# Kernel tuning notes

Hardware: AMD Instinct MI355X
Metric: run time of the kernel (lower is better)

Reference implementation:

```python
import jax, jax.numpy as jnp
import numpy as np

D_MODEL = 1024
NUM_ATOMS = 16384
TEMPERATURE = 1.0
NEG_INF = -1e9


def setup_inputs() -> dict:
    key = jax.random.key(0)
    kx, kd, km = jax.random.split(key, 3)
    x = jax.random.normal(kx, (4, 2048, D_MODEL), dtype=jnp.float32)
    # xavier_uniform for [num_atoms, d_model]
    limit = float(np.sqrt(6.0 / (NUM_ATOMS + D_MODEL)))
    dictionary = jax.random.uniform(
        kd, (NUM_ATOMS, D_MODEL), dtype=jnp.float32, minval=-limit, maxval=limit
    )
    mask = jax.random.randint(km, (4, 2048, NUM_ATOMS), 0, 2, dtype=jnp.int32)
    return {"x": x, "dictionary": dictionary, "mask": mask}


def reference(x, dictionary, mask):
    # scores: [b, s, num_atoms]
    scores = jnp.einsum("bsd,ad->bsa", x, dictionary)
    m = mask.astype(scores.dtype)
    scores = scores * m + (1.0 - m) * NEG_INF
    weights = jax.nn.softmax(scores / TEMPERATURE, axis=-1)
    reconstruction = jnp.einsum("bsa,ad->bsd", weights, dictionary)
    argmax_indices = jnp.argmax(scores, axis=-1)
    return reconstruction, argmax_indices
```

## Files before the change

### kernel.cpp

```cpp
#include <hip/hip_runtime.h>

#define NTOK   8192
#define DMODEL 1024
#define NATOM  16384

typedef _Float16 half8  __attribute__((ext_vector_type(8)));
typedef _Float16 half4_t __attribute__((ext_vector_type(4)));
typedef float    f32x4  __attribute__((ext_vector_type(4)));

#define GLOAD_LDS16(gsrc, ldst) \
  __builtin_amdgcn_global_load_lds((const __attribute__((address_space(1))) unsigned int*)(gsrc), \
                                   (__attribute__((address_space(3))) unsigned int*)(ldst), 16, 0, 0)

__global__ void cvt_f32_f16(const float* __restrict__ in, _Float16* __restrict__ out, int n4) {
  int i = blockIdx.x * 256 + threadIdx.x;
  if (i >= n4) return;
  float4 v = ((const float4*)in)[i];
  half4_t h;
  h[0] = (_Float16)v.x; h[1] = (_Float16)v.y; h[2] = (_Float16)v.z; h[3] = (_Float16)v.w;
  ((half4_t*)out)[i] = h;
}

__global__ void transpose_dict(const float* __restrict__ dict,
                               _Float16* __restrict__ Dh, _Float16* __restrict__ dT) {
  __shared__ _Float16 tile[64][68];
  int a0 = blockIdx.x * 64;
  int d0 = blockIdx.y * 64;
  int tid = threadIdx.x;
  int c = tid & 63;
  int r0 = tid >> 6;
  #pragma unroll
  for (int i = 0; i < 16; i++) {
    int r = r0 + i * 4;
    _Float16 h = (_Float16)dict[(size_t)(a0 + r) * DMODEL + d0 + c];
    tile[r][c] = h;
    Dh[(size_t)(a0 + r) * DMODEL + d0 + c] = h;
  }
  __syncthreads();
  #pragma unroll
  for (int i = 0; i < 16; i++) {
    int rd = r0 + i * 4;
    dT[(size_t)(d0 + rd) * NATOM + a0 + c] = tile[c][rd];
  }
}

__global__ void zero_lsum(float* __restrict__ lsum) {
  lsum[blockIdx.x * 256 + threadIdx.x] = 0.0f;
}

__device__ __forceinline__ void stage_ab(const _Float16* __restrict__ A,
                                         const _Float16* __restrict__ B,
                                         _Float16* As, _Float16* Bs,
                                         size_t arow0, size_t brow0, size_t ldk,
                                         int k0, int tid) {
  #pragma unroll
  for (int i = 0; i < 2; i++) {
    int L = tid + i * 256;
    int r = L >> 2, pc = L & 3;
    int c = pc ^ ((r >> 1) & 3);
    GLOAD_LDS16(A + (arow0 + r) * ldk + k0 + c * 8, As + (size_t)L * 8);
    GLOAD_LDS16(B + (brow0 + r) * ldk + k0 + c * 8, Bs + (size_t)L * 8);
  }
}

__launch_bounds__(256, 2)
__global__ void score_kernel(const _Float16* __restrict__ Xh,
                             const _Float16* __restrict__ Dh,
                             const int* __restrict__ mask,
                             _Float16* __restrict__ E,
                             float* __restrict__ lsum,
                             _Float16* __restrict__ Tmax) {
  __shared__ _Float16 lds[32768];
  const int tid  = threadIdx.x;
  const int lane = tid & 63;
  const int wave = tid >> 6;
  const int wm = wave >> 1, wn = wave & 1;
  const int swz = (blockIdx.x & 7) * 1024 + (blockIdx.x >> 3);
  const int nt = swz & 127;
  const int n0 = nt * 128;
  const int m0 = (swz >> 7) * 128;

  const int frow = lane & 15;
  const int fkc  = lane >> 4;

  f32x4 acc[4][4] = {};

  stage_ab(Xh, Dh, lds,         lds + 4096,  m0, n0, DMODEL, 0,  tid);
  stage_ab(Xh, Dh, lds + 8192,  lds + 12288, m0, n0, DMODEL, 32, tid);
  stage_ab(Xh, Dh, lds + 16384, lds + 20480, m0, n0, DMODEL, 64, tid);

  for (int t = 0; t < 32; ++t) {
    if (t < 30)       asm volatile("s_waitcnt vmcnt(8)" ::: "memory");
    else if (t == 30) asm volatile("s_waitcnt vmcnt(4)" ::: "memory");
    else              asm volatile("s_waitcnt vmcnt(0)" ::: "memory");
    __builtin_amdgcn_s_barrier();
    __builtin_amdgcn_sched_barrier(0);
    const _Float16* As = lds + (t & 3) * 8192;
    const _Float16* Bs = As + 4096;
    half8 af[4], bf[4];
    #pragma unroll
    for (int i = 0; i < 4; i++) {
      int ar = wm * 64 + i * 16 + frow;
      int br = wn * 64 + i * 16 + frow;
      af[i] = *(const half8*)&As[ar * 32 + ((fkc ^ ((ar >> 1) & 3)) << 3)];
      bf[i] = *(const half8*)&Bs[br * 32 + ((fkc ^ ((br >> 1) & 3)) << 3)];
    }
    if (t + 3 < 32) {
      int b = (t + 3) & 3;
      stage_ab(Xh, Dh, lds + b * 8192, lds + b * 8192 + 4096, m0, n0, DMODEL, (t + 3) * 32, tid);
    }
    __builtin_amdgcn_s_setprio(1);
    #pragma unroll
    for (int i = 0; i < 4; i++)
      #pragma unroll
      for (int j = 0; j < 4; j++)
        acc[i][j] = __builtin_amdgcn_mfma_f32_16x16x32_f16(af[i], bf[j], acc[i][j], 0, 0, 0);
    __builtin_amdgcn_s_setprio(0);
    __builtin_amdgcn_sched_barrier(0);
  }

  __syncthreads();
  const int cr = (lane >> 4) * 4;
  const int cc = lane & 15;
  #pragma unroll
  for (int i = 0; i < 4; i++) {
    #pragma unroll
    for (int j = 0; j < 4; j++) {
      #pragma unroll
      for (int r = 0; r < 4; r++) {
        int lr = wm * 64 + i * 16 + cr + r;
        int lc = wn * 64 + j * 16 + cc;
        int mk = mask[(size_t)(m0 + lr) * NATOM + (n0 + lc)];
        float e = mk ? __expf(acc[i][j][r]) : 0.0f;
        lds[lr * 136 + lc] = (_Float16)e;
      }
    }
  }
  __syncthreads();
  #pragma unroll
  for (int i = 0; i < 8; i++) {
    int chunk = i * 256 + tid;
    int r  = chunk >> 4;
    int c8 = (chunk & 15) * 8;
    *(half8*)&E[(size_t)(m0 + r) * NATOM + n0 + c8] = *(const half8*)&lds[r * 136 + c8];
  }
  {
    int r = tid >> 1, h = tid & 1;
    const _Float16* rowp = &lds[r * 136 + h * 64];
    float s = 0.0f, m = 0.0f;
    #pragma unroll
    for (int i = 0; i < 8; i++) {
      half8 v = *(const half8*)&rowp[i * 8];
      #pragma unroll
      for (int j = 0; j < 8; j++) { float f = (float)v[j]; s += f; m = fmaxf(m, f); }
    }
    s += __shfl_xor(s, 1, 64);
    m = fmaxf(m, __shfl_xor(m, 1, 64));
    if (h == 0) {
      atomicAdd(&lsum[m0 + r], s);
      Tmax[(size_t)nt * NTOK + m0 + r] = (_Float16)m;
    }
  }
}

__global__ void scan_lite(const _Float16* __restrict__ E,
                          const _Float16* __restrict__ Tmax,
                          const float* __restrict__ x,
                          const float* __restrict__ dict,
                          float* __restrict__ argout) {
  const int t = blockIdx.x;
  const int lane = threadIdx.x;
  float m0 = (float)Tmax[(size_t)lane * NTOK + t];
  float m1 = (float)Tmax[(size_t)(64 + lane) * NTOK + t];
  float mx = fmaxf(m0, m1);
  #pragma unroll
  for (int off = 32; off > 0; off >>= 1) mx = fmaxf(mx, __shfl_xor(mx, off, 64));

  __shared__ int cnt;
  __shared__ int cand[32];
  __shared__ double csc[32];
  if (lane == 0) cnt = 0;
  __syncthreads();

  if (mx > 0.0f) {
    float thr = 0.98f * mx;
    unsigned long long q0 = __ballot(m0 >= thr);
    unsigned long long q1 = __ballot(m1 >= thr);
    while (q0 | q1) {
      int tile;
      if (q0) { tile = __ffsll(q0) - 1; q0 &= q0 - 1; }
      else    { tile = 64 + __ffsll(q1) - 1; q1 &= q1 - 1; }
      const _Float16* ep = E + (size_t)t * NATOM + tile * 128;
      float e0 = (float)ep[lane], e1 = (float)ep[64 + lane];
      if (e0 >= thr) { int p = atomicAdd(&cnt, 1); if (p < 32) cand[p] = tile * 128 + lane; }
      if (e1 >= thr) { int p = atomicAdd(&cnt, 1); if (p < 32) cand[p] = tile * 128 + 64 + lane; }
    }
  }
  __syncthreads();
  int nc = min(cnt, 32);
  const float* xr = x + (size_t)t * DMODEL;
  for (int c = 0; c < nc; c++) {
    const float* dr = dict + (size_t)cand[c] * DMODEL;
    double a = 0.0;
    #pragma unroll
    for (int i = 0; i < 16; i++) {
      int d = lane + i * 64;
      a += (double)xr[d] * (double)dr[d];
    }
    #pragma unroll
    for (int off = 32; off > 0; off >>= 1) a += __shfl_down(a, off, 64);
    if (lane == 0) csc[c] = a;
  }
  __syncthreads();
  if (lane == 0) {
    int best = 0;
    if (nc > 0) {
      double bs = -1e300;
      best = NATOM;
      for (int c = 0; c < nc; c++)
        if (csc[c] > bs || (csc[c] == bs && cand[c] < best)) { bs = csc[c]; best = cand[c]; }
    }
    argout[t] = (float)best;
  }
}

__launch_bounds__(256, 2)
__global__ void recon_kernel(const _Float16* __restrict__ E,
                             const _Float16* __restrict__ DT,
                             const float* __restrict__ lsum,
                             float* __restrict__ out) {
  __shared__ _Float16 lds[32768];
  const int tid  = threadIdx.x;
  const int lane = tid & 63;
  const int wave = tid >> 6;
  const int wm = wave >> 1, wn = wave & 1;
  const int swz = (blockIdx.x & 7) * 64 + (blockIdx.x >> 3);
  const int n0 = (swz & 7) * 128;
  const int m0 = (swz >> 3) * 128;

  const int frow = lane & 15;
  const int fkc  = lane >> 4;

  f32x4 acc[4][4] = {};

  stage_ab(E, DT, lds,         lds + 4096,  m0, n0, NATOM, 0,  tid);
  stage_ab(E, DT, lds + 8192,  lds + 12288, m0, n0, NATOM, 32, tid);
  stage_ab(E, DT, lds + 16384, lds + 20480, m0, n0, NATOM, 64, tid);

  for (int t = 0; t < 512; ++t) {
    if (t < 510)       asm volatile("s_waitcnt vmcnt(8)" ::: "memory");
    else if (t == 510) asm volatile("s_waitcnt vmcnt(4)" ::: "memory");
    else               asm volatile("s_waitcnt vmcnt(0)" ::: "memory");
    __builtin_amdgcn_s_barrier();
    __builtin_amdgcn_sched_barrier(0);
    const _Float16* As = lds + (t & 3) * 8192;
    const _Float16* Bs = As + 4096;
    half8 af[4], bf[4];
    #pragma unroll
    for (int i = 0; i < 4; i++) {
      int ar = wm * 64 + i * 16 + frow;
      int br = wn * 64 + i * 16 + frow;
      af[i] = *(const half8*)&As[ar * 32 + ((fkc ^ ((ar >> 1) & 3)) << 3)];
      bf[i] = *(const half8*)&Bs[br * 32 + ((fkc ^ ((br >> 1) & 3)) << 3)];
    }
    if (t + 3 < 512) {
      int b = (t + 3) & 3;
      stage_ab(E, DT, lds + b * 8192, lds + b * 8192 + 4096, m0, n0, NATOM, (t + 3) * 32, tid);
    }
    __builtin_amdgcn_s_setprio(1);
    #pragma unroll
    for (int i = 0; i < 4; i++)
      #pragma unroll
      for (int j = 0; j < 4; j++)
        acc[i][j] = __builtin_amdgcn_mfma_f32_16x16x32_f16(af[i], bf[j], acc[i][j], 0, 0, 0);
    __builtin_amdgcn_s_setprio(0);
    __builtin_amdgcn_sched_barrier(0);
  }

  const int cr = (lane >> 4) * 4;
  const int cc = lane & 15;
  #pragma unroll
  for (int i = 0; i < 4; i++) {
    #pragma unroll
    for (int r = 0; r < 4; r++) {
      int lr = wm * 64 + i * 16 + cr + r;
      float sc = 1.0f / lsum[m0 + lr];
      #pragma unroll
      for (int j = 0; j < 4; j++) {
        int lc = wn * 64 + j * 16 + cc;
        out[(size_t)(m0 + lr) * DMODEL + (n0 + lc)] = acc[i][j][r] * sc;
      }
    }
  }
}

extern "C" void kernel_launch(void* const* d_in, const int* in_sizes, int n_in,
                              void* d_out, int out_size, void* d_ws, size_t ws_size,
                              hipStream_t stream) {
  const float* x    = (const float*)d_in[0];
  const float* dict = (const float*)d_in[1];
  const int*   mask = (const int*)d_in[2];
  float* recon  = (float*)d_out;
  float* argout = recon + (size_t)NTOK * DMODEL;

  char* w = (char*)d_ws;
  _Float16* Xh = (_Float16*)(w);
  _Float16* Dh = (_Float16*)(w + (size_t)16  * 1024 * 1024);
  _Float16* DT = (_Float16*)(w + (size_t)48  * 1024 * 1024);
  _Float16* E  = (_Float16*)(w + (size_t)80  * 1024 * 1024);
  float*  lsum = (float*)  (w + (size_t)336 * 1024 * 1024);
  _Float16* Tmax = (_Float16*)d_out;

  cvt_f32_f16<<<dim3(NTOK * DMODEL / 4 / 256), 256, 0, stream>>>(x, Xh, NTOK * DMODEL / 4);
  transpose_dict<<<dim3(NATOM / 64, DMODEL / 64), 256, 0, stream>>>(dict, Dh, DT);
  zero_lsum<<<dim3(NTOK / 256), 256, 0, stream>>>(lsum);
  score_kernel<<<dim3(8192), 256, 0, stream>>>(Xh, Dh, mask, E, lsum, Tmax);
  scan_lite<<<dim3(NTOK), 64, 0, stream>>>(E, Tmax, x, dict, argout);
  recon_kernel<<<dim3(512), 256, 0, stream>>>(E, DT, lsum, recon);
}
```

Before: 1.439 ms.

## Simplify score GEMM to double buffering and pack four tokens per scan block

The score kernel drops its 4-stage async LDS pipeline, explicit vmcnt waits, priority hints and block swizzle. It now uses a plain 2-buffer loop with __syncthreads and a 2D grid, and shared memory shrinks to fit the epilogue tile. Tmax is stored token-major, so scan_lite reads each token's tile maxima contiguously. scan_lite handles four tokens per 256-thread block with per-wave shared state and no block barriers. The smaller pipeline cuts LDS use and complexity but gives less latency hiding in the dominant GEMM, and dropping the swizzle may hurt L2 reuse.

```diff
diff --git a/kernel.cpp b/kernel.cpp
--- a/kernel.cpp
+++ b/kernel.cpp
@@ -70,53 +70,42 @@
                              _Float16* __restrict__ E,
                              float* __restrict__ lsum,
                              _Float16* __restrict__ Tmax) {
-  __shared__ _Float16 lds[32768];
+  __shared__ _Float16 lds[17408];
   const int tid  = threadIdx.x;
   const int lane = tid & 63;
   const int wave = tid >> 6;
   const int wm = wave >> 1, wn = wave & 1;
-  const int swz = (blockIdx.x & 7) * 1024 + (blockIdx.x >> 3);
-  const int nt = swz & 127;
-  const int n0 = nt * 128;
-  const int m0 = (swz >> 7) * 128;
+  const int m0 = blockIdx.y * 128;
+  const int n0 = blockIdx.x * 128;
 
   const int frow = lane & 15;
   const int fkc  = lane >> 4;
 
   f32x4 acc[4][4] = {};
 
-  stage_ab(Xh, Dh, lds,         lds + 4096,  m0, n0, DMODEL, 0,  tid);
-  stage_ab(Xh, Dh, lds + 8192,  lds + 12288, m0, n0, DMODEL, 32, tid);
-  stage_ab(Xh, Dh, lds + 16384, lds + 20480, m0, n0, DMODEL, 64, tid);
-
-  for (int t = 0; t < 32; ++t) {
-    if (t < 30)       asm volatile("s_waitcnt vmcnt(8)" ::: "memory");
-    else if (t == 30) asm volatile("s_waitcnt vmcnt(4)" ::: "memory");
-    else              asm volatile("s_waitcnt vmcnt(0)" ::: "memory");
-    __builtin_amdgcn_s_barrier();
-    __builtin_amdgcn_sched_barrier(0);
-    const _Float16* As = lds + (t & 3) * 8192;
-    const _Float16* Bs = As + 4096;
+  stage_ab(Xh, Dh, lds, lds + 4096, m0, n0, DMODEL, 0, tid);
+  int cur = 0;
+  for (int it = 0; it < DMODEL / 32; ++it) {
+    __syncthreads();
+    if (it + 1 < DMODEL / 32)
+      stage_ab(Xh, Dh, lds + (cur ^ 1) * 8192, lds + (cur ^ 1) * 8192 + 4096,
+               m0, n0, DMODEL, (it + 1) * 32, tid);
+    _Float16* As = lds + cur * 8192;
+    _Float16* Bs = As + 4096;
     half8 af[4], bf[4];
     #pragma unroll
     for (int i = 0; i < 4; i++) {
       int ar = wm * 64 + i * 16 + frow;
       int br = wn * 64 + i * 16 + frow;
-      af[i] = *(const half8*)&As[ar * 32 + ((fkc ^ ((ar >> 1) & 3)) << 3)];
-      bf[i] = *(const half8*)&Bs[br * 32 + ((fkc ^ ((br >> 1) & 3)) << 3)];
-    }
-    if (t + 3 < 32) {
-      int b = (t + 3) & 3;
-      stage_ab(Xh, Dh, lds + b * 8192, lds + b * 8192 + 4096, m0, n0, DMODEL, (t + 3) * 32, tid);
-    }
-    __builtin_amdgcn_s_setprio(1);
+      af[i] = *(const half8*)&As[ar * 32 + (fkc ^ ((ar >> 1) & 3)) * 8];
+      bf[i] = *(const half8*)&Bs[br * 32 + (fkc ^ ((br >> 1) & 3)) * 8];
+    }
     #pragma unroll
     for (int i = 0; i < 4; i++)
       #pragma unroll
       for (int j = 0; j < 4; j++)
         acc[i][j] = __builtin_amdgcn_mfma_f32_16x16x32_f16(af[i], bf[j], acc[i][j], 0, 0, 0);
-    __builtin_amdgcn_s_setprio(0);
-    __builtin_amdgcn_sched_barrier(0);
+    cur ^= 1;
   }
 
   __syncthreads();
@@ -158,7 +147,7 @@
     m = fmaxf(m, __shfl_xor(m, 1, 64));
     if (h == 0) {
       atomicAdd(&lsum[m0 + r], s);
-      Tmax[(size_t)nt * NTOK + m0 + r] = (_Float16)m;
+      Tmax[(size_t)(m0 + r) * 128 + blockIdx.x] = (_Float16)m;
     }
   }
 }
@@ -168,19 +157,21 @@
                           const float* __restrict__ x,
                           const float* __restrict__ dict,
                           float* __restrict__ argout) {
-  const int t = blockIdx.x;
-  const int lane = threadIdx.x;
-  float m0 = (float)Tmax[(size_t)lane * NTOK + t];
-  float m1 = (float)Tmax[(size_t)(64 + lane) * NTOK + t];
+  const int wv   = threadIdx.x >> 6;
+  const int lane = threadIdx.x & 63;
+  const int t = blockIdx.x * 4 + wv;
+
+  __shared__ int    cnt[4];
+  __shared__ int    cand[4][32];
+  __shared__ double csc[4][32];
+  if (lane == 0) cnt[wv] = 0;
+
+  const _Float16* tm = Tmax + (size_t)t * 128;
+  float m0 = (float)tm[lane];
+  float m1 = (float)tm[64 + lane];
   float mx = fmaxf(m0, m1);
   #pragma unroll
   for (int off = 32; off > 0; off >>= 1) mx = fmaxf(mx, __shfl_xor(mx, off, 64));
-
-  __shared__ int cnt;
-  __shared__ int cand[32];
-  __shared__ double csc[32];
-  if (lane == 0) cnt = 0;
-  __syncthreads();
 
   if (mx > 0.0f) {
     float thr = 0.98f * mx;
@@ -192,15 +183,14 @@
       else    { tile = 64 + __ffsll(q1) - 1; q1 &= q1 - 1; }
       const _Float16* ep = E + (size_t)t * NATOM + tile * 128;
       float e0 = (float)ep[lane], e1 = (float)ep[64 + lane];
-      if (e0 >= thr) { int p = atomicAdd(&cnt, 1); if (p < 32) cand[p] = tile * 128 + lane; }
-      if (e1 >= thr) { int p = atomicAdd(&cnt, 1); if (p < 32) cand[p] = tile * 128 + 64 + lane; }
-    }
-  }
-  __syncthreads();
-  int nc = min(cnt, 32);
+      if (e0 >= thr) { int p = atomicAdd(&cnt[wv], 1); if (p < 32) cand[wv][p] = tile * 128 + lane; }
+      if (e1 >= thr) { int p = atomicAdd(&cnt[wv], 1); if (p < 32) cand[wv][p] = tile * 128 + 64 + lane; }
+    }
+  }
+  int nc = min(cnt[wv], 32);
   const float* xr = x + (size_t)t * DMODEL;
   for (int c = 0; c < nc; c++) {
-    const float* dr = dict + (size_t)cand[c] * DMODEL;
+    const float* dr = dict + (size_t)cand[wv][c] * DMODEL;
     double a = 0.0;
     #pragma unroll
     for (int i = 0; i < 16; i++) {
@@ -209,16 +199,15 @@
     }
     #pragma unroll
     for (int off = 32; off > 0; off >>= 1) a += __shfl_down(a, off, 64);
-    if (lane == 0) csc[c] = a;
-  }
-  __syncthreads();
+    if (lane == 0) csc[wv][c] = a;
+  }
   if (lane == 0) {
     int best = 0;
     if (nc > 0) {
       double bs = -1e300;
       best = NATOM;
       for (int c = 0; c < nc; c++)
-        if (csc[c] > bs || (csc[c] == bs && cand[c] < best)) { bs = csc[c]; best = cand[c]; }
+        if (csc[wv][c] > bs || (csc[wv][c] == bs && cand[wv][c] < best)) { bs = csc[wv][c]; best = cand[wv][c]; }
     }
     argout[t] = (float)best;
   }
@@ -314,7 +303,7 @@
   cvt_f32_f16<<<dim3(NTOK * DMODEL / 4 / 256), 256, 0, stream>>>(x, Xh, NTOK * DMODEL / 4);
   transpose_dict<<<dim3(NATOM / 64, DMODEL / 64), 256, 0, stream>>>(dict, Dh, DT);
   zero_lsum<<<dim3(NTOK / 256), 256, 0, stream>>>(lsum);
-  score_kernel<<<dim3(8192), 256, 0, stream>>>(Xh, Dh, mask, E, lsum, Tmax);
-  scan_lite<<<dim3(NTOK), 64, 0, stream>>>(E, Tmax, x, dict, argout);
+  score_kernel<<<dim3(NATOM / 128, NTOK / 128), 256, 0, stream>>>(Xh, Dh, mask, E, lsum, Tmax);
+  scan_lite<<<dim3(NTOK / 4), 256, 0, stream>>>(E, Tmax, x, dict, argout);
   recon_kernel<<<dim3(512), 256, 0, stream>>>(E, DT, lsum, recon);
 }
```

After: 1.426 ms. Within noise of the previous version (-0.9%).
